# Performance work log

Measured on AMD Instinct MI355X. Metric: run time of the kernel, lower is better.

The kernel has to match this reference:

```python
import jax, jax.numpy as jnp
import numpy as np
from jax import lax

SCORE_THRESHOLD = 0.001
IOU_THRESHOLD = 0.7
MAX_DETECTIONS = 300
PRE_NMS_TOPK = 1024      # standard pre-NMS candidate cap (torchvision/YOLO practice)
CLASS_OFFSET = 4096.0    # > max image coord, separates classes so cross-class IoU == 0
IMG = 640.0

B, N, C = 32, 8400, 80


def setup_inputs() -> dict:
    key = jax.random.key(0)
    kc, ks, kp = jax.random.split(key, 3)
    # well-formed boxes in [y1, x1, y2, x2] convention (matches repo's nms())
    tl = jax.random.uniform(kc, (B, N, 2), jnp.float32, 0.0, IMG - 1.0)   # (y1, x1)
    wh = jax.random.uniform(ks, (B, N, 2), jnp.float32, 4.0, 160.0)      # (h, w)
    boxes = jnp.concatenate([tl, jnp.minimum(tl + wh, IMG)], axis=-1)     # [B,N,4]
    scores = jax.random.uniform(kp, (B, N, C), jnp.float32)               # [B,N,C]
    return {"boxes": boxes, "scores": scores}


def _pairwise_iou(b):
    # b: [B,K,4] as [y1,x1,y2,x2]; +1 pixel convention per the repo's nms()
    y1, x1, y2, x2 = b[..., 0], b[..., 1], b[..., 2], b[..., 3]
    areas = (x2 - x1 + 1.0) * (y2 - y1 + 1.0)                             # [B,K]
    yy1 = jnp.maximum(y1[:, :, None], y1[:, None, :])
    xx1 = jnp.maximum(x1[:, :, None], x1[:, None, :])
    yy2 = jnp.minimum(y2[:, :, None], y2[:, None, :])
    xx2 = jnp.minimum(x2[:, :, None], x2[:, None, :])
    w = jnp.maximum(0.0, xx2 - xx1 + 1.0)
    h = jnp.maximum(0.0, yy2 - yy1 + 1.0)
    inter = w * h                                                          # [B,K,K]
    return inter / (areas[:, :, None] + areas[:, None, :] - inter)


def multiclass_nms(boxes, scores):
    b, n, c = scores.shape
    flat = jnp.where(scores > SCORE_THRESHOLD, scores, 0.0).reshape(b, n * c)
    top_scores, top_idx = lax.top_k(flat, PRE_NMS_TOPK)                    # [B,K]
    box_idx = top_idx // c
    cls_idx = top_idx % c                                                  # int32 [B,K]
    cand = jnp.take_along_axis(boxes, box_idx[..., None], axis=1)          # [B,K,4]
    # offset boxes by class so per-class NMS happens in one shared pass
    off = cand + (cls_idx.astype(cand.dtype) * CLASS_OFFSET)[..., None]
    iou = _pairwise_iou(off)                                               # [B,K,K]

    k = PRE_NMS_TOPK
    idx = jnp.arange(k)
    keep0 = top_scores > SCORE_THRESHOLD                                   # [B,K]

    def body(i, keep):
        row = iou[:, i, :]                                                 # [B,K]
        sup = (row > IOU_THRESHOLD) & keep[:, i][:, None] & (idx[None, :] > i)
        return keep & ~sup

    keep = lax.fori_loop(0, k, body, keep0)                                # greedy NMS

    final_scores = jnp.where(keep, top_scores, 0.0)
    out_scores, sel = lax.top_k(final_scores, MAX_DETECTIONS)              # [B,300]
    out_boxes = jnp.take_along_axis(cand, sel[..., None], axis=1)          # [B,300,4]
    out_labels = jnp.take_along_axis(cls_idx, sel, axis=1)                 # [B,300]
    n_valid = jnp.minimum(jnp.sum(keep, axis=1, keepdims=True), MAX_DETECTIONS)
    return out_boxes, out_scores, out_labels.astype(jnp.int32), n_valid.astype(jnp.int32)


def reference(boxes, scores):
    return multiclass_nms(boxes, scores)
```

## Files before the change

### kernel.cpp

```cpp
#include <hip/hip_runtime.h>
#include <cstdint>
#include <cstddef>

#define B_      32
#define N_      8400
#define C_      80
#define NC      672000
#define NCV4    168000
#define NBINS   4096
#define TOPK    1024
#define MAXDET  300
#define CANDCAP 4096
#define NSLICE  16
#define SLICE_V4 10500
#define NBKT    8
#define SEGB    64
#define BSORT   256
#define CLS_CAP 256

#define STAGE_THRESH 0.998046875f

#define WS_SEGKEYS  0
#define WS_SEGCNT   2097152

#define OUT_SCORES  38400
#define OUT_LABELS  48000
#define OUT_NVALID  57600

__global__ __launch_bounds__(256) void stage_kernel(const float4* __restrict__ scores4,
                                                    unsigned* __restrict__ segCnt,
                                                    unsigned long long* __restrict__ segKeys) {
    __shared__ unsigned lcnt[NBKT];
    int b = blockIdx.x, sl = blockIdx.y, tid = threadIdx.x;
    if (tid < NBKT) lcnt[tid] = 0;
    __syncthreads();
    const float4* s = scores4 + (size_t)b * NCV4 + (size_t)sl * SLICE_V4;
    for (int i = tid; i < SLICE_V4; i += 256) {
        float4 v = s[i];
        float c[4] = {v.x, v.y, v.z, v.w};
        unsigned flat0 = ((unsigned)sl * SLICE_V4 + (unsigned)i) * 4u;
        #pragma unroll
        for (int kc = 0; kc < 4; ++kc) {
            float x = (c[kc] > 0.001f) ? c[kc] : 0.0f;
            if (x >= STAGE_THRESH) {
                int bin = (int)(x * 4096.0f);
                bin = bin > (NBINS - 1) ? (NBINS - 1) : bin;
                int bkt = bin - 4088;
                unsigned p = atomicAdd(&lcnt[bkt], 1u);
                if (p < (unsigned)SEGB)
                    segKeys[(((size_t)(b * NBKT + bkt)) * NSLICE + sl) * SEGB + p] =
                        ((unsigned long long)__float_as_uint(x) << 32) |
                        (unsigned long long)(0xFFFFFFFFu - (flat0 + kc));
            }
        }
    }
    __syncthreads();
    if (tid < NBKT) segCnt[(b * NBKT + tid) * NSLICE + sl] = lcnt[tid];
}

__global__ __launch_bounds__(1024) void fused_kernel(
        const float4* __restrict__ scores4,
        const unsigned long long* __restrict__ segKeys,
        const unsigned* __restrict__ segCnt,
        const float4* __restrict__ boxes4,
        float* __restrict__ out) {
    __shared__ unsigned scnt2[NBKT * NSLICE];
    __shared__ unsigned bsum[NBKT];
    __shared__ unsigned bok[NBKT];
    __shared__ unsigned spref[NBKT][NSLICE];
    __shared__ float   sScore[TOPK];
    __shared__ int     sBoxIdx[TOPK];
    __shared__ __align__(16) unsigned char sClsv[TOPK];
    __shared__ float4  sBox[TOPK];
    __shared__ unsigned char sKeep[TOPK];
    __shared__ unsigned short sposW[16][CLS_CAP];
    __shared__ unsigned char  supW[16][CLS_CAP];
    __shared__ int wsum[16];
    __shared__ int sel[MAXDET];
    __shared__ int s_cut;
    __shared__ unsigned s_scnt;
    __shared__ __align__(16) char upool[49152];
    unsigned long long* kbuf = (unsigned long long*)upool;
    unsigned* fh = (unsigned*)(upool + 32768);

    int b = blockIdx.x, tid = threadIdx.x;
    int lane = tid & 63, wave = tid >> 6;

    if (tid < NBKT * NSLICE) scnt2[tid] = segCnt[b * NBKT * NSLICE + tid];
    __syncthreads();
    if (tid < NBKT) {
        unsigned ssum = 0, ok = 1;
        #pragma unroll
        for (int sl = 0; sl < NSLICE; ++sl) {
            unsigned v = scnt2[tid * NSLICE + sl];
            if (v > (unsigned)SEGB) ok = 0;
            ssum += v;
        }
        bsum[tid] = ssum; bok[tid] = ok;
    }
    if (tid < NBKT * NSLICE) {
        int bkt = tid >> 4, sl = tid & 15;
        unsigned acc = 0;
        for (int s2 = 0; s2 < sl; ++s2) acc += scnt2[bkt * NSLICE + s2];
        spref[bkt][sl] = acc;
    }
    __syncthreads();
    unsigned M = 0; int valid = 1;
    #pragma unroll
    for (int t = 0; t < NBKT; ++t) {
        unsigned s2 = bsum[t];
        if (!bok[t] || s2 > (unsigned)BSORT) valid = 0;
        M += s2;
    }
    if (M < (unsigned)TOPK || M > (unsigned)CANDCAP) valid = 0;

    if (valid) {
        for (int seg = wave; seg < NBKT * NSLICE; seg += 16) {
            int bkt = seg >> 4, sl = seg & 15;
            unsigned c2 = scnt2[seg];
            if ((unsigned)lane < c2)
                kbuf[bkt * BSORT + spref[bkt][sl] + lane] =
                    segKeys[(((size_t)(b * NBKT + bkt)) * NSLICE + sl) * SEGB + lane];
        }
        __syncthreads();
        int bkt = tid >> 7;
        unsigned n = bsum[bkt];
        unsigned base = 0;
        for (int t = bkt + 1; t < NBKT; ++t) base += bsum[t];
        if (base < (unsigned)TOPK && n > 0) {
            const unsigned long long* kb = kbuf + bkt * BSORT;
            int j0 = tid & 127, j1 = j0 + 128;
            unsigned long long k0 = (j0 < (int)n) ? kb[j0] : 0ull;
            unsigned long long k1 = (j1 < (int)n) ? kb[j1] : 0ull;
            unsigned r0 = 0, r1 = 0;
            for (unsigned i = 0; i < n; ++i) {
                unsigned long long ki = kb[i];
                r0 += (ki > k0); r1 += (ki > k1);
            }
            if (j0 < (int)n) {
                unsigned pos = base + r0;
                if (pos < (unsigned)TOPK) {
                    unsigned idx = 0xFFFFFFFFu - (unsigned)(k0 & 0xFFFFFFFFull);
                    if (idx >= (unsigned)NC) idx = 0;
                    unsigned bi = idx / (unsigned)C_;
                    sScore[pos] = __uint_as_float((unsigned)(k0 >> 32));
                    sClsv[pos] = (unsigned char)(0x80u | (idx - bi * (unsigned)C_));
                    sBoxIdx[pos] = (int)bi;
                }
            }
            if (j1 < (int)n) {
                unsigned pos = base + r1;
                if (pos < (unsigned)TOPK) {
                    unsigned idx = 0xFFFFFFFFu - (unsigned)(k1 & 0xFFFFFFFFull);
                    if (idx >= (unsigned)NC) idx = 0;
                    unsigned bi = idx / (unsigned)C_;
                    sScore[pos] = __uint_as_float((unsigned)(k1 >> 32));
                    sClsv[pos] = (unsigned char)(0x80u | (idx - bi * (unsigned)C_));
                    sBoxIdx[pos] = (int)bi;
                }
            }
        }
    } else {
        for (int i = tid; i < NBINS; i += 1024) fh[i] = 0;
        if (tid == 0) s_scnt = 0;
        __syncthreads();
        const float4* s = scores4 + (size_t)b * NCV4;
        for (int i = tid; i < NCV4; i += 1024) {
            float4 v = s[i];
            float c4[4] = {v.x, v.y, v.z, v.w};
            #pragma unroll
            for (int kc = 0; kc < 4; ++kc) {
                float x = (c4[kc] > 0.001f) ? c4[kc] : 0.0f;
                int bin = (int)(x * 4096.0f);
                bin = bin > (NBINS - 1) ? (NBINS - 1) : bin;
                atomicAdd(&fh[bin], 1u);
            }
        }
        __syncthreads();
        if (tid == 0) {
            unsigned acc = 0; int cb2 = 0;
            for (int bin = NBINS - 1; bin >= 0; --bin) {
                acc += fh[bin];
                if (acc >= (unsigned)TOPK) { cb2 = bin; break; }
            }
            s_cut = cb2;
        }
        __syncthreads();
        int cb = s_cut;
        for (int i = tid; i < NCV4; i += 1024) {
            float4 v = s[i];
            float c4[4] = {v.x, v.y, v.z, v.w};
            unsigned flat0 = (unsigned)i * 4u;
            #pragma unroll
            for (int kc = 0; kc < 4; ++kc) {
                float x = (c4[kc] > 0.001f) ? c4[kc] : 0.0f;
                int bin = (int)(x * 4096.0f);
                bin = bin > (NBINS - 1) ? (NBINS - 1) : bin;
                if (bin >= cb) {
                    unsigned p = atomicAdd(&s_scnt, 1u);
                    if (p < (unsigned)CANDCAP)
                        kbuf[p] = ((unsigned long long)__float_as_uint(x) << 32) |
                                  (unsigned long long)(0xFFFFFFFFu - (flat0 + kc));
                }
            }
        }
        __syncthreads();
        unsigned M2 = s_scnt; if (M2 > (unsigned)CANDCAP) M2 = CANDCAP;
        int S = (M2 <= 1024u) ? 1024 : (M2 <= 2048u ? 2048 : CANDCAP);
        for (int i = (int)M2 + tid; i < S; i += 1024) kbuf[i] = 0ull;
        __syncthreads();
        for (int kk = 2; kk <= S; kk <<= 1) {
            for (int j = kk >> 1; j > 0; j >>= 1) {
                for (int t = tid; t < S; t += 1024) {
                    int l = t ^ j;
                    if (l > t) {
                        unsigned long long a0 = kbuf[t], c0 = kbuf[l];
                        bool sw = ((t & kk) == 0) ? (a0 < c0) : (a0 > c0);
                        if (sw) { kbuf[t] = c0; kbuf[l] = a0; }
                    }
                }
                __syncthreads();
            }
        }
        for (int r = tid; r < TOPK; r += 1024) {
            unsigned long long key = kbuf[r];
            float sc = __uint_as_float((unsigned)(key >> 32));
            unsigned idx = 0xFFFFFFFFu - (unsigned)(key & 0xFFFFFFFFull);
            if (idx >= (unsigned)NC) idx = 0;
            unsigned bi = idx / (unsigned)C_;
            sScore[r] = sc;
            sClsv[r] = (unsigned char)((sc > 0.001f ? 0x80u : 0u) |
                                       (idx - bi * (unsigned)C_));
            sBoxIdx[r] = (int)bi;
        }
    }
    __syncthreads();

    sBox[tid] = boxes4[(size_t)b * N_ + sBoxIdx[tid]];
    sKeep[tid] = 0;
    __syncthreads();

    for (int c = wave; c < C_; c += 16) {
        unsigned target = 0x80u | (unsigned)c;
        unsigned d0 = ((const unsigned*)sClsv)[lane * 4 + 0];
        unsigned d1 = ((const unsigned*)sClsv)[lane * 4 + 1];
        unsigned d2 = ((const unsigned*)sClsv)[lane * 4 + 2];
        unsigned d3 = ((const unsigned*)sClsv)[lane * 4 + 3];
        unsigned mmask = 0; int cnt = 0;
        #pragma unroll
        for (int t = 0; t < 16; ++t) {
            unsigned d = (t < 4) ? d0 : (t < 8) ? d1 : (t < 12) ? d2 : d3;
            unsigned v = (d >> ((t & 3) * 8)) & 0xffu;
            if (v == target) { mmask |= (1u << t); ++cnt; }
        }
        int x = cnt;
        #pragma unroll
        for (int o = 1; o < 64; o <<= 1) {
            int y = __shfl_up(x, o, 64);
            if (lane >= o) x += y;
        }
        int pre = x - cnt;
        int m = __shfl(x, 63, 64);
        int slot = pre;
        #pragma unroll
        for (int t = 0; t < 16; ++t) {
            if ((mmask >> t) & 1u) {
                if (slot < CLS_CAP) sposW[wave][slot] = (unsigned short)(lane * 16 + t);
                ++slot;
            }
        }
        int m2 = m < CLS_CAP ? m : CLS_CAP;
        __threadfence_block();
        float off = (float)c * 4096.0f;
        if (m2 <= 64) {
            float y1 = 0, x1 = 0, y2 = 0, x2 = 0, ar = 0; int p = 0;
            if (lane < m2) {
                p = sposW[wave][lane];
                float4 tb = sBox[p];
                y1 = tb.x + off; x1 = tb.y + off;
                y2 = tb.z + off; x2 = tb.w + off;
                ar = __fmul_rn((x2 - x1) + 1.0f, (y2 - y1) + 1.0f);
            }
            unsigned long long sup = 0, keepm = 0;
            for (int i = 0; i < m2; ++i) {
                if ((sup >> i) & 1ull) continue;
                keepm |= 1ull << i;
                float cy1 = __shfl(y1, i, 64), cx1 = __shfl(x1, i, 64);
                float cy2 = __shfl(y2, i, 64), cx2 = __shfl(x2, i, 64);
                float ca  = __shfl(ar, i, 64);
                bool over = false;
                if (lane < m2 && lane > i) {
                    float yy1 = fmaxf(cy1, y1), xx1 = fmaxf(cx1, x1);
                    float yy2 = fminf(cy2, y2), xx2 = fminf(cx2, x2);
                    float w2 = fmaxf(0.0f, (xx2 - xx1) + 1.0f);
                    float h2 = fmaxf(0.0f, (yy2 - yy1) + 1.0f);
                    float inter = __fmul_rn(w2, h2);
                    float denom = (ca + ar) - inter;
                    over = inter / denom > 0.7f;
                }
                sup |= __ballot(over);
            }
            if (lane < m2 && ((keepm >> lane) & 1ull)) sKeep[p] = 1;
        } else {
            for (int j = lane; j < m2; j += 64) supW[wave][j] = 0;
            __threadfence_block();
            int cur = 0;
            while (cur < m2) {
                int pc = sposW[wave][cur];
                if (lane == 0) sKeep[pc] = 1;
                float4 cb4 = sBox[pc];
                float cy1 = cb4.x + off, cx1 = cb4.y + off;
                float cy2 = cb4.z + off, cx2 = cb4.w + off;
                float ca = __fmul_rn((cx2 - cx1) + 1.0f, (cy2 - cy1) + 1.0f);
                for (int j = cur + 1 + lane; j < m2; j += 64) {
                    if (!supW[wave][j]) {
                        float4 tb = sBox[sposW[wave][j]];
                        float y1 = tb.x + off, x1 = tb.y + off;
                        float y2 = tb.z + off, x2 = tb.w + off;
                        float arj = __fmul_rn((x2 - x1) + 1.0f, (y2 - y1) + 1.0f);
                        float yy1 = fmaxf(cy1, y1), xx1 = fmaxf(cx1, x1);
                        float yy2 = fminf(cy2, y2), xx2 = fminf(cx2, x2);
                        float w2 = fmaxf(0.0f, (xx2 - xx1) + 1.0f);
                        float h2 = fmaxf(0.0f, (yy2 - yy1) + 1.0f);
                        float inter = __fmul_rn(w2, h2);
                        float denom = (ca + arj) - inter;
                        if (inter / denom > 0.7f) supW[wave][j] = 1;
                    }
                }
                __threadfence_block();
                int nxt = m2;
                for (int j = cur + 1 + lane; j < m2; j += 64)
                    if (!supW[wave][j]) { nxt = j; break; }
                for (int o = 32; o > 0; o >>= 1) {
                    int other = __shfl_xor(nxt, o, 64);
                    nxt = nxt < other ? nxt : other;
                }
                cur = nxt;
            }
        }
    }
    __syncthreads();

    int kp = sKeep[tid];
    unsigned long long mb = __ballot(kp != 0);
    int wpre = __popcll(mb & ((1ull << lane) - 1ull));
    if (lane == 0) wsum[wave] = __popcll(mb);
    __syncthreads();
    int wbase = 0, nk = 0;
    #pragma unroll
    for (int t = 0; t < 16; ++t) {
        int v = wsum[t];
        if (t < wave) wbase += v;
        nk += v;
    }
    int kexcl = wbase + wpre;
    int sexcl = tid - kexcl;
    if (kp) {
        if (kexcl < MAXDET) sel[kexcl] = tid;
    } else {
        int slot2 = nk + sexcl;
        if (slot2 < MAXDET) sel[slot2] = tid;
    }
    __syncthreads();
    if (tid < MAXDET) {
        int p = sel[tid];
        float sc = (tid < nk) ? sScore[p] : 0.0f;
        float4 tb = sBox[p];
        float* ob = out + ((size_t)b * MAXDET + tid) * 4;
        ob[0] = tb.x; ob[1] = tb.y; ob[2] = tb.z; ob[3] = tb.w;
        out[OUT_SCORES + b * MAXDET + tid] = sc;
        out[OUT_LABELS + b * MAXDET + tid] = (float)(sClsv[p] & 0x7f);
    }
    if (tid == 0) out[OUT_NVALID + b] = (float)(nk < MAXDET ? nk : MAXDET);
}

extern "C" void kernel_launch(void* const* d_in, const int* in_sizes, int n_in,
                              void* d_out, int out_size, void* d_ws, size_t ws_size,
                              hipStream_t stream) {
    const float* boxes  = (const float*)d_in[0];
    const float* scores = (const float*)d_in[1];
    float* out = (float*)d_out;
    char* ws = (char*)d_ws;

    unsigned long long* segKeys = (unsigned long long*)(ws + WS_SEGKEYS);
    unsigned* segCnt = (unsigned*)(ws + WS_SEGCNT);

    const float4* scores4 = (const float4*)scores;
    const float4* boxes4  = (const float4*)boxes;

    stage_kernel<<<dim3(B_, NSLICE), 256, 0, stream>>>(scores4, segCnt, segKeys);
    fused_kernel<<<B_, 1024, 0, stream>>>(scores4, segKeys, segCnt, boxes4, out);
}
```

Measured before the change: 181.9 us.

## Split per-class NMS into a separate class-parallel kernel across many blocks

Adds an nms_direct_kernel launched on a grid of 32 images by 20 groups of 4 classes. Each wave gathers its class's candidates, computes their top-K rank by counting within the score bucket, and runs greedy NMS for that class, writing scores, boxes, class ids and keep flags to workspace. The finalize kernel then only compacts keep flags into the output on the fast path, and keeps the old single-block path as a fallback. This spreads the serial NMS work from 32 blocks to 640 blocks, at the cost of an extra launch, redundant candidate loading in every block and a round trip through global memory.

Result: slower. 186.6 us (+2.6%).

```diff
diff --git a/kernel.cpp b/kernel.cpp
--- a/kernel.cpp
+++ b/kernel.cpp
@@ -16,12 +16,18 @@
 #define NBKT    8
 #define SEGB    64
 #define BSORT   256
-#define CLS_CAP 256
+#define MTIGHT  2048
+#define CAND_CAP 256
+#define NMSD_CPB 4
 
 #define STAGE_THRESH 0.998046875f
 
 #define WS_SEGKEYS  0
 #define WS_SEGCNT   2097152
+#define WS_TOPSCORE 2113536
+#define WS_TOPBOX   2244608
+#define WS_CLSV     2768896
+#define WS_KEEP     2801664
 
 #define OUT_SCORES  38400
 #define OUT_LABELS  48000
@@ -58,25 +64,277 @@
     if (tid < NBKT) segCnt[(b * NBKT + tid) * NSLICE + sl] = lcnt[tid];
 }
 
-__global__ __launch_bounds__(1024) void fused_kernel(
+__global__ __launch_bounds__(256) void nms_direct_kernel(
+        const unsigned long long* __restrict__ segKeys,
+        const unsigned* __restrict__ segCnt,
+        const float4* __restrict__ boxes4,
+        float* __restrict__ topScore,
+        float4* __restrict__ topBox4,
+        unsigned char* __restrict__ clsv,
+        unsigned char* __restrict__ keepB) {
+    __shared__ unsigned sCnt[NBKT * NSLICE];
+    __shared__ unsigned sPref[NBKT * NSLICE];
+    __shared__ unsigned sBStart[NBKT], sBCnt[NBKT], sBase[NBKT];
+    __shared__ unsigned kLo[MTIGHT], kHi[MTIGHT];
+    __shared__ unsigned short wCand[NMSD_CPB][CAND_CAP];
+    __shared__ unsigned short wPos[NMSD_CPB][CAND_CAP];
+    __shared__ unsigned short wOPos[NMSD_CPB][CAND_CAP];
+    __shared__ float wy1[NMSD_CPB][CAND_CAP], wx1[NMSD_CPB][CAND_CAP];
+    __shared__ float wy2[NMSD_CPB][CAND_CAP], wx2[NMSD_CPB][CAND_CAP];
+    __shared__ float war[NMSD_CPB][CAND_CAP];
+    __shared__ unsigned char wSup[NMSD_CPB][CAND_CAP];
+
+    int b = blockIdx.x, g = blockIdx.y, tid = threadIdx.x;
+    int lane = tid & 63, wave = tid >> 6;
+
+    if (tid < NBKT * NSLICE) sCnt[tid] = segCnt[b * NBKT * NSLICE + tid];
+    __syncthreads();
+    unsigned M = 0; int valid = 1; unsigned bsumR[NBKT];
+    #pragma unroll
+    for (int t = 0; t < NBKT; ++t) {
+        unsigned s2 = 0, mx = 0;
+        #pragma unroll
+        for (int sl = 0; sl < NSLICE; ++sl) {
+            unsigned v = sCnt[t * NSLICE + sl];
+            s2 += v; mx = v > mx ? v : mx;
+        }
+        if (mx > (unsigned)SEGB || s2 > (unsigned)BSORT) valid = 0;
+        bsumR[t] = s2; M += s2;
+    }
+    if (M < (unsigned)TOPK || M > (unsigned)MTIGHT) valid = 0;
+    if (!valid) return;
+    if (tid < NBKT * NSLICE) {
+        unsigned a = 0;
+        for (int i = 0; i < tid; ++i) a += sCnt[i];
+        sPref[tid] = a;
+    }
+    if (tid < NBKT) {
+        unsigned st = 0, ba = 0;
+        for (int t = 0; t < tid; ++t) st += bsumR[t];
+        for (int t = tid + 1; t < NBKT; ++t) ba += bsumR[t];
+        sBStart[tid] = st; sBCnt[tid] = bsumR[tid]; sBase[tid] = ba;
+    }
+    __syncthreads();
+
+    #pragma unroll 4
+    for (int s32 = 0; s32 < 32; ++s32) {
+        int seg = wave * 32 + s32;
+        unsigned k = sCnt[seg], off = sPref[seg];
+        const unsigned long long* src =
+            segKeys + ((size_t)b * NBKT * NSLICE + seg) * SEGB;
+        if ((unsigned)lane < k) {
+            unsigned long long v = src[lane];
+            kLo[off + lane] = (unsigned)v;
+            kHi[off + lane] = (unsigned)(v >> 32);
+        }
+    }
+    __syncthreads();
+
+    int c = g * NMSD_CPB + wave;
+    float offc = (float)c * 4096.0f;
+    unsigned mc = 0;
+    for (unsigned r0 = 0; r0 < M; r0 += 64) {
+        unsigned i = r0 + lane; bool match = false;
+        if (i < M) {
+            unsigned flat = ~kLo[i];
+            if (flat >= (unsigned)NC) flat = 0;
+            unsigned cls = flat % (unsigned)C_;
+            match = (cls == (unsigned)c);
+        }
+        unsigned long long mb = __ballot(match);
+        int pre = __popcll(mb & ((1ull << lane) - 1ull));
+        if (match) {
+            unsigned s = mc + pre;
+            if (s < (unsigned)CAND_CAP) wCand[wave][s] = (unsigned short)i;
+        }
+        mc += (unsigned)__popcll(mb);
+    }
+    if (mc > (unsigned)CAND_CAP) mc = CAND_CAP;
+    __threadfence_block();
+    if (mc == 0) return;
+
+    if (mc <= 64) {
+        unsigned short mypos = 0xFFFF;
+        float y1 = 0, x1 = 0, y2 = 0, x2 = 0, ar = 0;
+        if (lane < (int)mc) {
+            unsigned i = wCand[wave][lane];
+            unsigned lo = kLo[i], hi = kHi[i];
+            float sc = __uint_as_float(hi);
+            int bin = (int)(sc * 4096.0f);
+            bin = bin > (NBINS - 1) ? (NBINS - 1) : bin;
+            int bkt = bin - 4088;
+            bkt = bkt < 0 ? 0 : (bkt > 7 ? 7 : bkt);
+            unsigned st = sBStart[bkt], nb = sBCnt[bkt], r = 0;
+            for (unsigned t = 0; t < nb; ++t) {
+                unsigned oh = kHi[st + t];
+                if (oh > hi || (oh == hi && kLo[st + t] > lo)) ++r;
+            }
+            unsigned pos = sBase[bkt] + r;
+            unsigned flat = ~lo;
+            if (flat >= (unsigned)NC) flat = 0;
+            unsigned bi = flat / (unsigned)C_;
+            if (pos < (unsigned)TOPK) {
+                float4 tb = boxes4[(size_t)b * N_ + bi];
+                topScore[b * TOPK + pos] = sc;
+                topBox4[(size_t)b * TOPK + pos] = tb;
+                clsv[(size_t)b * TOPK + pos] = (unsigned char)(0x80u | c);
+                mypos = (unsigned short)pos;
+                y1 = tb.x + offc; x1 = tb.y + offc;
+                y2 = tb.z + offc; x2 = tb.w + offc;
+                ar = __fmul_rn((x2 - x1) + 1.0f, (y2 - y1) + 1.0f);
+            }
+        }
+        wPos[wave][lane] = mypos;
+        __threadfence_block();
+        bool vme = (lane < (int)mc) && (mypos != 0xFFFF);
+        int srank = 0;
+        for (unsigned k2 = 0; k2 < mc; ++k2) {
+            unsigned short pk = wPos[wave][k2];
+            if (pk != 0xFFFF && pk < mypos) ++srank;
+        }
+        int mc2 = (int)__popcll(__ballot(vme));
+        if (vme) {
+            wy1[wave][srank] = y1; wx1[wave][srank] = x1;
+            wy2[wave][srank] = y2; wx2[wave][srank] = x2;
+            war[wave][srank] = ar; wOPos[wave][srank] = mypos;
+        }
+        __threadfence_block();
+        float Y1 = 0, X1 = 0, Y2 = 0, X2 = 0, AR = 0; unsigned short OP = 0;
+        if (lane < mc2) {
+            Y1 = wy1[wave][lane]; X1 = wx1[wave][lane];
+            Y2 = wy2[wave][lane]; X2 = wx2[wave][lane];
+            AR = war[wave][lane]; OP = wOPos[wave][lane];
+        }
+        unsigned long long sup = 0, keepm = 0;
+        for (int i = 0; i < mc2; ++i) {
+            if ((sup >> i) & 1ull) continue;
+            keepm |= 1ull << i;
+            float cy1 = __shfl(Y1, i, 64), cx1 = __shfl(X1, i, 64);
+            float cy2 = __shfl(Y2, i, 64), cx2 = __shfl(X2, i, 64);
+            float ca  = __shfl(AR, i, 64);
+            bool over = false;
+            if (lane < mc2 && lane > i) {
+                float yy1 = fmaxf(cy1, Y1), xx1 = fmaxf(cx1, X1);
+                float yy2 = fminf(cy2, Y2), xx2 = fminf(cx2, X2);
+                float w2 = fmaxf(0.0f, (xx2 - xx1) + 1.0f);
+                float h2 = fmaxf(0.0f, (yy2 - yy1) + 1.0f);
+                float inter = __fmul_rn(w2, h2);
+                float denom = (ca + AR) - inter;
+                over = inter / denom > 0.7f;
+            }
+            sup |= __ballot(over);
+        }
+        if (lane < mc2)
+            keepB[(size_t)b * TOPK + OP] = (unsigned char)((keepm >> lane) & 1ull);
+    } else {
+        for (unsigned j = lane; j < mc; j += 64) {
+            unsigned i = wCand[wave][j];
+            unsigned lo = kLo[i], hi = kHi[i];
+            float sc = __uint_as_float(hi);
+            int bin = (int)(sc * 4096.0f);
+            bin = bin > (NBINS - 1) ? (NBINS - 1) : bin;
+            int bkt = bin - 4088;
+            bkt = bkt < 0 ? 0 : (bkt > 7 ? 7 : bkt);
+            unsigned st = sBStart[bkt], nb = sBCnt[bkt], r = 0;
+            for (unsigned t = 0; t < nb; ++t) {
+                unsigned oh = kHi[st + t];
+                if (oh > hi || (oh == hi && kLo[st + t] > lo)) ++r;
+            }
+            unsigned pos = sBase[bkt] + r;
+            unsigned flat = ~lo;
+            if (flat >= (unsigned)NC) flat = 0;
+            unsigned bi = flat / (unsigned)C_;
+            unsigned short ps = 0xFFFF;
+            if (pos < (unsigned)TOPK) {
+                float4 tb = boxes4[(size_t)b * N_ + bi];
+                topScore[b * TOPK + pos] = sc;
+                topBox4[(size_t)b * TOPK + pos] = tb;
+                clsv[(size_t)b * TOPK + pos] = (unsigned char)(0x80u | c);
+                ps = (unsigned short)pos;
+            }
+            wPos[wave][j] = ps;
+        }
+        for (unsigned j = mc + lane; j < (unsigned)CAND_CAP; j += 64)
+            wPos[wave][j] = 0xFFFF;
+        __threadfence_block();
+        int mc2 = 0;
+        for (unsigned k2 = 0; k2 < mc; ++k2)
+            if (wPos[wave][k2] != 0xFFFF) ++mc2;
+        for (unsigned j = lane; j < mc; j += 64) {
+            unsigned short pj = wPos[wave][j];
+            if (pj != 0xFFFF) {
+                int sr = 0;
+                for (unsigned k2 = 0; k2 < mc; ++k2) {
+                    unsigned short pk = wPos[wave][k2];
+                    if (pk != 0xFFFF && pk < pj) ++sr;
+                }
+                unsigned i = wCand[wave][j];
+                unsigned flat = ~kLo[i];
+                if (flat >= (unsigned)NC) flat = 0;
+                unsigned bi = flat / (unsigned)C_;
+                float4 tb = boxes4[(size_t)b * N_ + bi];
+                float y1 = tb.x + offc, x1 = tb.y + offc;
+                float y2 = tb.z + offc, x2 = tb.w + offc;
+                wy1[wave][sr] = y1; wx1[wave][sr] = x1;
+                wy2[wave][sr] = y2; wx2[wave][sr] = x2;
+                war[wave][sr] = __fmul_rn((x2 - x1) + 1.0f, (y2 - y1) + 1.0f);
+                wOPos[wave][sr] = pj; wSup[wave][sr] = 0;
+            }
+        }
+        __threadfence_block();
+        int cur = 0;
+        while (cur < mc2) {
+            float cy1 = wy1[wave][cur], cx1 = wx1[wave][cur];
+            float cy2 = wy2[wave][cur], cx2 = wx2[wave][cur];
+            float ca = war[wave][cur];
+            for (int j = cur + 1 + lane; j < mc2; j += 64) {
+                if (!wSup[wave][j]) {
+                    float yy1 = fmaxf(cy1, wy1[wave][j]), xx1 = fmaxf(cx1, wx1[wave][j]);
+                    float yy2 = fminf(cy2, wy2[wave][j]), xx2 = fminf(cx2, wx2[wave][j]);
+                    float w2 = fmaxf(0.0f, (xx2 - xx1) + 1.0f);
+                    float h2 = fmaxf(0.0f, (yy2 - yy1) + 1.0f);
+                    float inter = __fmul_rn(w2, h2);
+                    float denom = (ca + war[wave][j]) - inter;
+                    if (inter / denom > 0.7f) wSup[wave][j] = 1;
+                }
+            }
+            __threadfence_block();
+            int nxt = mc2;
+            for (int j = cur + 1 + lane; j < mc2; j += 64)
+                if (!wSup[wave][j]) { nxt = j; break; }
+            for (int o = 32; o > 0; o >>= 1) {
+                int other = __shfl_xor(nxt, o, 64);
+                nxt = nxt < other ? nxt : other;
+            }
+            cur = nxt;
+        }
+        for (int j = lane; j < mc2; j += 64)
+            keepB[(size_t)b * TOPK + wOPos[wave][j]] = wSup[wave][j] ? 0 : 1;
+    }
+}
+
+__global__ __launch_bounds__(1024) void finalize_kernel(
         const float4* __restrict__ scores4,
         const unsigned long long* __restrict__ segKeys,
         const unsigned* __restrict__ segCnt,
         const float4* __restrict__ boxes4,
+        const float* __restrict__ topScore,
+        const float4* __restrict__ topBox4,
+        const unsigned char* __restrict__ clsv,
+        const unsigned char* __restrict__ keepB,
         float* __restrict__ out) {
     __shared__ unsigned scnt2[NBKT * NSLICE];
+    __shared__ int wsum[16];
+    __shared__ int sel[MAXDET];
     __shared__ unsigned bsum[NBKT];
-    __shared__ unsigned bok[NBKT];
-    __shared__ unsigned spref[NBKT][NSLICE];
+    __shared__ unsigned spref2[NBKT][NSLICE];
     __shared__ float   sScore[TOPK];
     __shared__ int     sBoxIdx[TOPK];
     __shared__ __align__(16) unsigned char sClsv[TOPK];
     __shared__ float4  sBox[TOPK];
     __shared__ unsigned char sKeep[TOPK];
-    __shared__ unsigned short sposW[16][CLS_CAP];
-    __shared__ unsigned char  supW[16][CLS_CAP];
-    __shared__ int wsum[16];
-    __shared__ int sel[MAXDET];
+    __shared__ unsigned short sposW[16][BSORT];
+    __shared__ unsigned char  supW[16][BSORT];
     __shared__ int s_cut;
     __shared__ unsigned s_scnt;
     __shared__ __align__(16) char upool[49152];
@@ -88,38 +346,84 @@
 
     if (tid < NBKT * NSLICE) scnt2[tid] = segCnt[b * NBKT * NSLICE + tid];
     __syncthreads();
-    if (tid < NBKT) {
-        unsigned ssum = 0, ok = 1;
+    unsigned M = 0; int valid = 1; unsigned bsumR[NBKT];
+    #pragma unroll
+    for (int t = 0; t < NBKT; ++t) {
+        unsigned s2 = 0, mx = 0;
         #pragma unroll
         for (int sl = 0; sl < NSLICE; ++sl) {
-            unsigned v = scnt2[tid * NSLICE + sl];
-            if (v > (unsigned)SEGB) ok = 0;
-            ssum += v;
-        }
-        bsum[tid] = ssum; bok[tid] = ok;
-    }
+            unsigned v = scnt2[t * NSLICE + sl];
+            s2 += v; mx = v > mx ? v : mx;
+        }
+        if (mx > (unsigned)SEGB || s2 > (unsigned)BSORT) valid = 0;
+        bsumR[t] = s2; M += s2;
+    }
+    if (M < (unsigned)TOPK || M > (unsigned)MTIGHT) valid = 0;
+
+    if (valid) {
+        int kp = keepB[(size_t)b * TOPK + tid];
+        unsigned long long mb = __ballot(kp != 0);
+        int wpre = __popcll(mb & ((1ull << lane) - 1ull));
+        if (lane == 0) wsum[wave] = __popcll(mb);
+        __syncthreads();
+        int wbase = 0, nk = 0;
+        #pragma unroll
+        for (int t = 0; t < 16; ++t) {
+            int v = wsum[t];
+            if (t < wave) wbase += v;
+            nk += v;
+        }
+        int kexcl = wbase + wpre;
+        int sexcl = tid - kexcl;
+        if (kp) {
+            if (kexcl < MAXDET) sel[kexcl] = tid;
+        } else {
+            int slot2 = nk + sexcl;
+            if (slot2 < MAXDET) sel[slot2] = tid;
+        }
+        __syncthreads();
+        if (tid < MAXDET) {
+            int p = sel[tid];
+            float sc = (tid < nk) ? topScore[b * TOPK + p] : 0.0f;
+            float4 tb = topBox4[(size_t)b * TOPK + p];
+            float* ob = out + ((size_t)b * MAXDET + tid) * 4;
+            ob[0] = tb.x; ob[1] = tb.y; ob[2] = tb.z; ob[3] = tb.w;
+            out[OUT_SCORES + b * MAXDET + tid] = sc;
+            out[OUT_LABELS + b * MAXDET + tid] =
+                (float)(clsv[(size_t)b * TOPK + p] & 0x7f);
+        }
+        if (tid == 0) out[OUT_NVALID + b] = (float)(nk < MAXDET ? nk : MAXDET);
+        return;
+    }
+
     if (tid < NBKT * NSLICE) {
         int bkt = tid >> 4, sl = tid & 15;
         unsigned acc = 0;
         for (int s2 = 0; s2 < sl; ++s2) acc += scnt2[bkt * NSLICE + s2];
-        spref[bkt][sl] = acc;
-    }
-    __syncthreads();
-    unsigned M = 0; int valid = 1;
+        spref2[bkt][sl] = acc;
+        if (sl == 0) bsum[bkt] = bsumR[bkt];
+    }
+    __syncthreads();
+    int valid2 = 1; unsigned M2c = 0;
     #pragma unroll
     for (int t = 0; t < NBKT; ++t) {
-        unsigned s2 = bsum[t];
-        if (!bok[t] || s2 > (unsigned)BSORT) valid = 0;
-        M += s2;
-    }
-    if (M < (unsigned)TOPK || M > (unsigned)CANDCAP) valid = 0;
-
-    if (valid) {
+        unsigned s2 = 0, mx = 0;
+        #pragma unroll
+        for (int sl = 0; sl < NSLICE; ++sl) {
+            unsigned v = scnt2[t * NSLICE + sl];
+            s2 += v; mx = v > mx ? v : mx;
+        }
+        if (mx > (unsigned)SEGB || s2 > (unsigned)BSORT) valid2 = 0;
+        M2c += s2;
+    }
+    if (M2c < (unsigned)TOPK || M2c > (unsigned)CANDCAP) valid2 = 0;
+
+    if (valid2) {
         for (int seg = wave; seg < NBKT * NSLICE; seg += 16) {
             int bkt = seg >> 4, sl = seg & 15;
             unsigned c2 = scnt2[seg];
             if ((unsigned)lane < c2)
-                kbuf[bkt * BSORT + spref[bkt][sl] + lane] =
+                kbuf[bkt * BSORT + spref2[bkt][sl] + lane] =
                     segKeys[(((size_t)(b * NBKT + bkt)) * NSLICE + sl) * SEGB + lane];
         }
         __syncthreads();
@@ -205,9 +509,9 @@
             }
         }
         __syncthreads();
-        unsigned M2 = s_scnt; if (M2 > (unsigned)CANDCAP) M2 = CANDCAP;
-        int S = (M2 <= 1024u) ? 1024 : (M2 <= 2048u ? 2048 : CANDCAP);
-        for (int i = (int)M2 + tid; i < S; i += 1024) kbuf[i] = 0ull;
+        unsigned Mf = s_scnt; if (Mf > (unsigned)CANDCAP) Mf = CANDCAP;
+        int S = (Mf <= 1024u) ? 1024 : (Mf <= 2048u ? 2048 : CANDCAP);
+        for (int i = (int)Mf + tid; i < S; i += 1024) kbuf[i] = 0ull;
         __syncthreads();
         for (int kk = 2; kk <= S; kk <<= 1) {
             for (int j = kk >> 1; j > 0; j >>= 1) {
@@ -235,11 +539,9 @@
         }
     }
     __syncthreads();
-
     sBox[tid] = boxes4[(size_t)b * N_ + sBoxIdx[tid]];
     sKeep[tid] = 0;
     __syncthreads();
-
     for (int c = wave; c < C_; c += 16) {
         unsigned target = 0x80u | (unsigned)c;
         unsigned d0 = ((const unsigned*)sClsv)[lane * 4 + 0];
@@ -265,11 +567,11 @@
         #pragma unroll
         for (int t = 0; t < 16; ++t) {
             if ((mmask >> t) & 1u) {
-                if (slot < CLS_CAP) sposW[wave][slot] = (unsigned short)(lane * 16 + t);
+                if (slot < BSORT) sposW[wave][slot] = (unsigned short)(lane * 16 + t);
                 ++slot;
             }
         }
-        int m2 = m < CLS_CAP ? m : CLS_CAP;
+        int m2 = m < BSORT ? m : BSORT;
         __threadfence_block();
         float off = (float)c * 4096.0f;
         if (m2 <= 64) {
@@ -340,7 +642,6 @@
         }
     }
     __syncthreads();
-
     int kp = sKeep[tid];
     unsigned long long mb = __ballot(kp != 0);
     int wpre = __popcll(mb & ((1ull << lane) - 1ull));
@@ -384,10 +685,17 @@
 
     unsigned long long* segKeys = (unsigned long long*)(ws + WS_SEGKEYS);
     unsigned* segCnt = (unsigned*)(ws + WS_SEGCNT);
+    float* topScore = (float*)(ws + WS_TOPSCORE);
+    float4* topBox4 = (float4*)(ws + WS_TOPBOX);
+    unsigned char* clsv = (unsigned char*)(ws + WS_CLSV);
+    unsigned char* keepB = (unsigned char*)(ws + WS_KEEP);
 
     const float4* scores4 = (const float4*)scores;
     const float4* boxes4  = (const float4*)boxes;
 
     stage_kernel<<<dim3(B_, NSLICE), 256, 0, stream>>>(scores4, segCnt, segKeys);
-    fused_kernel<<<B_, 1024, 0, stream>>>(scores4, segKeys, segCnt, boxes4, out);
+    nms_direct_kernel<<<dim3(B_, C_ / NMSD_CPB), 256, 0, stream>>>(
+        segKeys, segCnt, boxes4, topScore, topBox4, clsv, keepB);
+    finalize_kernel<<<B_, 1024, 0, stream>>>(scores4, segKeys, segCnt, boxes4,
+                                             topScore, topBox4, clsv, keepB, out);
 }
```
